# Performance work log

Hardware: AMD Instinct MI355X
Metric: run time of the kernel (lower is better)

Reference implementation:

```python
import jax, jax.numpy as jnp
import numpy as np
import math

BATCH = 32
F_IN, F_OUT = 16, 32
B_IN, B_OUT = 16, 8
N_SPEC = B_OUT * (4 * B_OUT ** 2 - 1) // 3  # sum_{l<b_out} (2l+1)^2 = 680
ALPHAS = [2.0 * np.pi * a / 6.0 for a in range(6)]
GAMMAS = [2.0 * np.pi * c / 4.0 for c in range(4)]
GRID = [(al, np.pi / 16.0, ga) for al in ALPHAS for ga in GAMMAS]  # 24 (alpha, beta, gamma) points
SCALING = 1.0 / math.sqrt(len(GRID) * F_IN * B_OUT ** 3 / B_IN ** 3)


def _wigner_d(l, beta):
    """Wigner small-d matrix d^l_{m'm}(beta), centered order m',m=-l..l, quantum/Condon-Shortley."""
    lg = math.lgamma
    cb, sb = math.cos(beta / 2.0), math.sin(beta / 2.0)
    d = np.zeros((2 * l + 1, 2 * l + 1))
    for i, mp in enumerate(range(-l, l + 1)):
        for j, m in enumerate(range(-l, l + 1)):
            pref = 0.5 * (lg(l + mp + 1) + lg(l - mp + 1) + lg(l + m + 1) + lg(l - m + 1))
            tot = 0.0
            for s in range(max(0, m - mp), min(l + m, l - mp) + 1):
                den = lg(l + m - s + 1) + lg(s + 1) + lg(mp - m + s + 1) + lg(l - mp - s + 1)
                tot += ((-1.0) ** (mp - m + s) * math.exp(pref - den)
                        * cb ** (2 * l + m - mp - 2 * s) * sb ** (mp - m + 2 * s))
            d[i, j] = tot
    return d


def _quad_weights(b):
    """SOFT quadrature weights at beta_j = pi(2j+1)/(4b); 1/(2b)^2 absorbs the unnormalized 2D FFT."""
    k = np.arange(b)
    j = np.arange(2 * b)
    w = (2.0 / b) * np.sin(np.pi * (2 * j + 1) / (4.0 * b)) * (
        np.sin(np.pi * np.outer(2 * j + 1, 2 * k + 1) / (4.0 * b)) / (2 * k + 1)).sum(axis=1)
    return w / (2 * b) ** 2


def _setup_tables():
    betas_in = np.pi * (2 * np.arange(2 * B_IN) + 1) / (4.0 * B_IN)
    betas_out = np.pi * (2 * np.arange(2 * B_OUT) + 1) / (4.0 * B_OUT)
    w = _quad_weights(B_IN)
    wig_fwd = np.stack([np.concatenate([w[j] * _wigner_d(l, b).ravel() for l in range(B_OUT)])
                        for j, b in enumerate(betas_in)])          # [2*B_IN, N_SPEC]
    wig_inv = np.stack([np.concatenate([(2 * l + 1) * _wigner_d(l, b).ravel() for l in range(B_OUT)])
                        for b in betas_out])                       # [2*B_OUT, N_SPEC]
    F = np.zeros((len(GRID), N_SPEC), dtype=np.complex128)
    for p, (al, be, ga) in enumerate(GRID):
        blocks = []
        for l in range(B_OUT):
            m = np.arange(-l, l + 1)
            D = np.exp(-1j * m[:, None] * al) * _wigner_d(l, be) * np.exp(-1j * m[None, :] * ga)
            blocks.append(np.conj(D).ravel())
        F[p] = np.concatenate(blocks)
    return (wig_fwd.astype(np.float32), wig_inv.astype(np.float32),
            F.real.astype(np.float32), F.imag.astype(np.float32))


def _freq_idx(l, n):
    # packed frequencies -l..-1,0..l with wraparound into an FFT axis of length n
    return np.r_[np.arange(n - l, n), np.arange(l + 1)] if l > 0 else np.arange(1)


def _forward(x, kernel, bias, wigner_fwd, wigner_inv, ft_re, ft_im):
    xf = jnp.fft.fft2(x)  # FFT over (alpha, gamma): [B, Fin, 2b_in, 2b_in, 2b_in] complex64
    # SO3_fft_real: weighted Wigner-d contraction over beta, per degree l
    xhat = []
    for l in range(B_OUT):
        idx = _freq_idx(l, 2 * B_IN)
        xx = xf[:, :, :, idx[:, None], idx[None, :]]  # [B, Fin, beta, 2l+1, 2l+1]
        s0 = l * (4 * l * l - 1) // 3
        wl = wigner_fwd[:, s0:s0 + (2 * l + 1) ** 2].reshape(2 * B_IN, 2 * l + 1, 2 * l + 1)
        xhat.append(jnp.einsum('bmn,zfbmn->mnzf', wl, xx))  # [2l+1, 2l+1, B, Fin]
    # so3_rft of the scaled kernel on the grid: yhat [N_SPEC, Fin, Fout]
    Fc = ft_re + 1j * ft_im  # [P, N_SPEC]
    yhat = jnp.einsum('iop,ps->sio', (kernel * SCALING).astype(jnp.complex64), Fc)
    # so3_mm: per-degree z^l = x^l (y^l)^H, then inverse SO3 FFT
    B = x.shape[0]
    ff = jnp.zeros((B, F_OUT, 2 * B_OUT, 2 * B_OUT, 2 * B_OUT), dtype=xf.dtype)
    for l in range(B_OUT):
        s0 = l * (4 * l * l - 1) // 3
        yl = yhat[s0:s0 + (2 * l + 1) ** 2].reshape(2 * l + 1, 2 * l + 1, F_IN, F_OUT)
        zl = jnp.einsum('mkzf,nkfg->mnzg', xhat[l], jnp.conj(yl))  # [2l+1, 2l+1, B, Fout]
        wl = wigner_inv[:, s0:s0 + (2 * l + 1) ** 2].reshape(2 * B_OUT, 2 * l + 1, 2 * l + 1)
        o = jnp.einsum('mnzg,bmn->zgbmn', zl, wl)  # [B, Fout, beta_out, 2l+1, 2l+1]
        idx = _freq_idx(l, 2 * B_OUT)
        ff = ff.at[:, :, :, idx[:, None], idx[None, :]].add(o)
    out = jnp.real(jnp.fft.ifft2(ff)) * float((2 * B_OUT) ** 2)  # undo ifft 1/N^2, keep real part
    return out + bias


def setup_inputs():
    key = jax.random.key(0)
    k1, k2 = jax.random.split(key)
    x = jax.random.normal(k1, (BATCH, F_IN, 2 * B_IN, 2 * B_IN, 2 * B_IN), dtype=jnp.float32)
    kernel = jax.random.uniform(k2, (F_IN, F_OUT, len(GRID)), minval=-1.0, maxval=1.0, dtype=jnp.float32)
    bias = jnp.zeros((1, F_OUT, 1, 1, 1), jnp.float32)
    wf, wi, fre, fim = _setup_tables()
    return {"x": x, "kernel": kernel, "bias": bias,
            "wigner_fwd": jnp.asarray(wf), "wigner_inv": jnp.asarray(wi),
            "ft_re": jnp.asarray(fre), "ft_im": jnp.asarray(fim)}


def reference(x, kernel, bias, wigner_fwd, wigner_inv, ft_re, ft_im):
    return _forward(x, kernel, bias, wigner_fwd, wigner_inv, ft_re, ft_im)
```

## Files before the change

### kernel.cpp

```cpp
#include <hip/hip_runtime.h>
#include <math.h>


#define NS 680
#define NR 372
#define NP 24
#define NW 15
#define SLB 4
#define SCALING 0.14433756729740643f

__device__ __constant__ int c_s0[9] = {0, 1, 10, 35, 84, 165, 286, 455, 680};
__device__ __constant__ int c_o[9]  = {0, 1, 7, 22, 50, 95, 161, 252, 372};

__device__ __constant__ float2 TW32[32] = {
    { 1.0000000000f,  0.0000000000f}, { 0.9807852804f, -0.1950903220f},
    { 0.9238795325f, -0.3826834324f}, { 0.8314696123f, -0.5555702330f},
    { 0.7071067812f, -0.7071067812f}, { 0.5555702330f, -0.8314696123f},
    { 0.3826834324f, -0.9238795325f}, { 0.1950903220f, -0.9807852804f},
    { 0.0000000000f, -1.0000000000f}, {-0.1950903220f, -0.9807852804f},
    {-0.3826834324f, -0.9238795325f}, {-0.5555702330f, -0.8314696123f},
    {-0.7071067812f, -0.7071067812f}, {-0.8314696123f, -0.5555702330f},
    {-0.9238795325f, -0.3826834324f}, {-0.9807852804f, -0.1950903220f},
    {-1.0000000000f,  0.0000000000f}, {-0.9807852804f,  0.1950903220f},
    {-0.9238795325f,  0.3826834324f}, {-0.8314696123f,  0.5555702330f},
    {-0.7071067812f,  0.7071067812f}, {-0.5555702330f,  0.8314696123f},
    {-0.3826834324f,  0.9238795325f}, {-0.1950903220f,  0.9807852804f},
    { 0.0000000000f,  1.0000000000f}, { 0.1950903220f,  0.9807852804f},
    { 0.3826834324f,  0.9238795325f}, { 0.5555702330f,  0.8314696123f},
    { 0.7071067812f,  0.7071067812f}, { 0.8314696123f,  0.5555702330f},
    { 0.9238795325f,  0.3826834324f}, { 0.9807852804f,  0.1950903220f}};

__device__ __constant__ float2 TW16P[16] = {
    { 1.0000000000f,  0.0000000000f}, { 0.9238795325f,  0.3826834324f},
    { 0.7071067812f,  0.7071067812f}, { 0.3826834324f,  0.9238795325f},
    { 0.0000000000f,  1.0000000000f}, {-0.3826834324f,  0.9238795325f},
    {-0.7071067812f,  0.7071067812f}, {-0.9238795325f,  0.3826834324f},
    {-1.0000000000f,  0.0000000000f}, {-0.9238795325f, -0.3826834324f},
    {-0.7071067812f, -0.7071067812f}, {-0.3826834324f, -0.9238795325f},
    { 0.0000000000f, -1.0000000000f}, { 0.3826834324f, -0.9238795325f},
    { 0.7071067812f, -0.7071067812f}, { 0.9238795325f, -0.3826834324f}};

__global__ __launch_bounds__(256) void A12(const float* __restrict__ x,
                                           float2* __restrict__ xf2) {
    __shared__ __align__(16) float  sx[SLB * 1152];
    __shared__ __align__(16) float2 st[SLB][8][34];
    __shared__ float2 tw[32];
    int blk = blockIdx.x;
    int tid = threadIdx.x;
    if (tid < 32) tw[tid] = TW32[tid];
    {
        const float4* xs = (const float4*)(x + (size_t)blk * (SLB * 1024));
#pragma unroll
        for (int q = 0; q < SLB; q++) {
            int idx = q * 256 + tid;
            float4 v4 = xs[idx];
            int sl = idx >> 8, w = idx & 255;
            *(float4*)&sx[sl * 1152 + (w >> 3) * 36 + (w & 7) * 4] = v4;
        }
    }
    __syncthreads();
    {
        int u = tid >> 3, n = tid & 7;
        float sgn = (n & 1) ? -1.f : 1.f;
        float2 t8[8];
#pragma unroll
        for (int c = 0; c < 8; c++) t8[c] = tw[(n * c) & 31];
        float2 fa1 = tw[(8 * n) & 31];
#pragma unroll
        for (int sl = 0; sl < SLB; sl++) {
            const float* row = &sx[sl * 1152 + u * 36];
            float4 x0 = *(float4*)&row[0],  x1 = *(float4*)&row[4];
            float4 x2 = *(float4*)&row[8],  x3 = *(float4*)&row[12];
            float4 x4 = *(float4*)&row[16], x5 = *(float4*)&row[20];
            float4 x6 = *(float4*)&row[24], x7 = *(float4*)&row[28];
            float y0  = fmaf(sgn, x4.x, x0.x), y1  = fmaf(sgn, x4.y, x0.y);
            float y2  = fmaf(sgn, x4.z, x0.z), y3  = fmaf(sgn, x4.w, x0.w);
            float y4  = fmaf(sgn, x5.x, x1.x), y5  = fmaf(sgn, x5.y, x1.y);
            float y6  = fmaf(sgn, x5.z, x1.z), y7  = fmaf(sgn, x5.w, x1.w);
            float y8  = fmaf(sgn, x6.x, x2.x), y9  = fmaf(sgn, x6.y, x2.y);
            float y10 = fmaf(sgn, x6.z, x2.z), y11 = fmaf(sgn, x6.w, x2.w);
            float y12 = fmaf(sgn, x7.x, x3.x), y13 = fmaf(sgn, x7.y, x3.y);
            float y14 = fmaf(sgn, x7.z, x3.z), y15 = fmaf(sgn, x7.w, x3.w);
            float p0r = y0 * t8[0].x + y1 * t8[1].x + y2 * t8[2].x + y3 * t8[3].x
                      + y4 * t8[4].x + y5 * t8[5].x + y6 * t8[6].x + y7 * t8[7].x;
            float p0i = y0 * t8[0].y + y1 * t8[1].y + y2 * t8[2].y + y3 * t8[3].y
                      + y4 * t8[4].y + y5 * t8[5].y + y6 * t8[6].y + y7 * t8[7].y;
            float p1r = y8 * t8[0].x + y9 * t8[1].x + y10 * t8[2].x + y11 * t8[3].x
                      + y12 * t8[4].x + y13 * t8[5].x + y14 * t8[6].x + y15 * t8[7].x;
            float p1i = y8 * t8[0].y + y9 * t8[1].y + y10 * t8[2].y + y11 * t8[3].y
                      + y12 * t8[4].y + y13 * t8[5].y + y14 * t8[6].y + y15 * t8[7].y;
            float re = p0r + fa1.x * p1r - fa1.y * p1i;
            float im = p0i + fa1.x * p1i + fa1.y * p1r;
            st[sl][n][u] = make_float2(re, im);
        }
    }
    __syncthreads();
    {
        int sl = tid >> 6, m = (tid >> 3) & 7, jj = tid & 7;
        float2 t8[8], fa[4];
#pragma unroll
        for (int c = 0; c < 8; c++) t8[c] = tw[(m * c) & 31];
        fa[0] = make_float2(1.f, 0.f);
#pragma unroll
        for (int a = 1; a < 4; a++) fa[a] = tw[(8 * m * a) & 31];
        float reP = 0.f, imP = 0.f, reN = 0.f, imN = 0.f;
#pragma unroll
        for (int a = 0; a < 4; a++) {
            const float4* spt = (const float4*)&st[sl][jj][a * 8];
            float4 r0 = spt[0], r1 = spt[1], r2 = spt[2], r3 = spt[3];
            float A = r0.x * t8[0].x + r0.z * t8[1].x + r1.x * t8[2].x + r1.z * t8[3].x
                    + r2.x * t8[4].x + r2.z * t8[5].x + r3.x * t8[6].x + r3.z * t8[7].x;
            float B = r0.y * t8[0].y + r0.w * t8[1].y + r1.y * t8[2].y + r1.w * t8[3].y
                    + r2.y * t8[4].y + r2.w * t8[5].y + r3.y * t8[6].y + r3.w * t8[7].y;
            float C = r0.x * t8[0].y + r0.z * t8[1].y + r1.x * t8[2].y + r1.z * t8[3].y
                    + r2.x * t8[4].y + r2.z * t8[5].y + r3.x * t8[6].y + r3.z * t8[7].y;
            float D = r0.y * t8[0].x + r0.w * t8[1].x + r1.y * t8[2].x + r1.w * t8[3].x
                    + r2.y * t8[4].x + r2.w * t8[5].x + r3.y * t8[6].x + r3.w * t8[7].x;
            float prP = A - B, piP = C + D;
            float prN = A + B, piN = C - D;
            reP += fa[a].x * prP - fa[a].y * piP;
            imP += fa[a].x * piP + fa[a].y * prP;
            reN += fa[a].x * prN - fa[a].y * piN;
            imN += fa[a].x * piN + fa[a].y * prN;
        }
        int slice = blk * SLB + sl;
        float2* ob = xf2 + (size_t)slice * 120 + m * 15;
        ob[7 + jj] = make_float2(reP, imP);
        if (jj) ob[7 - jj] = make_float2(reN, imN);
    }
}

__global__ void kP(const float* __restrict__ kern, const float* __restrict__ fre,
                   const float* __restrict__ fim, const float* __restrict__ wf,
                   const float* __restrict__ wi, float2* __restrict__ yhat,
                   float* __restrict__ wfT, float* __restrict__ wiTd) {
    int idx = blockIdx.x * blockDim.x + threadIdx.x;
    if (idx < NS * 512) {
        int s = idx >> 9, fg = idx & 511;
        float re = 0.f, im = 0.f;
        for (int p = 0; p < NP; p++) {
            float kv = kern[fg * NP + p];
            re += kv * fre[p * NS + s];
            im += kv * fim[p * NS + s];
        }
        yhat[(size_t)s * 512 + fg] = make_float2(re * SCALING, im * SCALING);
        return;
    }
    int j = idx - NS * 512;
    if (j < NR * 32) {
        int sp = j >> 5, b = j & 31;
        int l = 0;
#pragma unroll
        for (int t = 1; t < 8; t++) if (sp >= c_o[t]) l = t;
        int K = 2 * l + 1, r = sp - c_o[l];
        int m = r / K, jn = r - m * K;
        int sf = c_s0[l] + (m + l) * K + jn;
        wfT[sp * 32 + b] = wf[b * NS + sf];
        return;
    }
    int k = j - NR * 32;
    if (k >= 16384) return;
    int ni = k & 15, mm = (k >> 4) & 7, b8 = (k >> 7) & 7;
    int l = (k >> 10) & 7, bh = k >> 13;
    int nn = ni - 7;
    float v = 0.f;
    if (ni < 15 && mm <= l && nn >= -l && nn <= l) {
        int K = 2 * l + 1;
        v = wi[(bh * 8 + b8) * NS + c_s0[l] + (mm + l) * K + (nn + l)];
    }
    wiTd[k] = v;
}

__global__ __launch_bounds__(256) void A3(const float2* __restrict__ xf2,
                                          const float* __restrict__ wfT,
                                          float2* __restrict__ xhat) {
    __shared__ __align__(16) float2 sxf[32 * 120];
    int zf = blockIdx.x;
    int tid = threadIdx.x;
    {
        const float4* src = (const float4*)(xf2 + (size_t)zf * (32 * 120));
        float4* dst = (float4*)sxf;
        for (int t = tid; t < 32 * 60; t += 256) dst[t] = src[t];
    }
    __syncthreads();
#pragma unroll
    for (int q = 0; q < 2; q++) {
        if (q == 1 && tid >= NR - 256) break;
        int sp = tid + q * 256;
        int l = 0;
#pragma unroll
        for (int t = 1; t < 8; t++) if (sp >= c_o[t]) l = t;
        int K = 2 * l + 1, r = sp - c_o[l];
        int m = r / K, jn = r - m * K;
        int cell = m * 15 + (jn - l + 7);
        const float4* wp = (const float4*)(wfT + sp * 32);
        const float2* xp = sxf + cell;
        float re = 0.f, im = 0.f;
#pragma unroll
        for (int qq = 0; qq < 8; qq++) {
            float4 w4 = wp[qq];
            float2 v0 = xp[(qq * 4 + 0) * 120];
            float2 v1 = xp[(qq * 4 + 1) * 120];
            float2 v2 = xp[(qq * 4 + 2) * 120];
            float2 v3 = xp[(qq * 4 + 3) * 120];
            re += w4.x * v0.x + w4.y * v1.x + w4.z * v2.x + w4.w * v3.x;
            im += w4.x * v0.y + w4.y * v1.y + w4.z * v2.y + w4.w * v3.y;
        }
        xhat[(size_t)sp * 512 + zf] = make_float2(re, im);
    }
}

__global__ __launch_bounds__(512) void kD(const float2* __restrict__ xhat,
                                          const float2* __restrict__ yhat,
                                          float2* __restrict__ zbufT) {
    __shared__ __align__(16) float2 Xs[4][16][34];
    __shared__ __align__(16) float2 Ys[4][16][34];
    int sp = 371 - blockIdx.x;
    int l = 0;
#pragma unroll
    for (int t = 1; t < 8; t++) if (sp >= c_o[t]) l = t;
    int K = 2 * l + 1, r = sp - c_o[l];
    int m = r / K, jn = r - m * K;
    int sX0 = c_o[l] + m * K;
    int sY0 = c_s0[l] + jn * K;
    int tid = threadIdx.x;
    int zl = tid >> 4;
    int g0 = (tid & 15) * 2;
    float2 acc0 = make_float2(0.f, 0.f), acc1 = make_float2(0.f, 0.f);
    int nchunks = (K + 3) >> 2;
    for (int chunk = 0; chunk < nchunks; ++chunk) {
#pragma unroll
        for (int kw = 0; kw < 4; kw++) {
            int k = chunk * 4 + kw;
            if (k < K)
                Xs[kw][tid & 15][tid >> 4] =
                    xhat[(size_t)(sX0 + k) * 512 + (tid >> 4) * 16 + (tid & 15)];
        }
#pragma unroll
        for (int kw = 0; kw < 4; kw++) {
            int k = chunk * 4 + kw;
            if (k < K)
                Ys[kw][tid >> 5][tid & 31] = yhat[(size_t)(sY0 + k) * 512 + tid];
        }
        __syncthreads();
#pragma unroll
        for (int kw = 0; kw < 4; kw++) {
            int k = chunk * 4 + kw;
            if (k < K) {
#pragma unroll
                for (int f = 0; f < 16; f++) {
                    float2 xv = Xs[kw][f][zl];
                    float4 y4 = *(const float4*)&Ys[kw][f][g0];
                    acc0.x += xv.x * y4.x + xv.y * y4.y;
                    acc0.y += xv.y * y4.x - xv.x * y4.y;
                    acc1.x += xv.x * y4.z + xv.y * y4.w;
                    acc1.y += xv.y * y4.z - xv.x * y4.w;
                }
            }
        }
        __syncthreads();
    }
    zbufT[(size_t)(zl * 32 + g0) * NR + sp]     = acc0;
    zbufT[(size_t)(zl * 32 + g0 + 1) * NR + sp] = acc1;
}

__global__ __launch_bounds__(256) void kE4(const float2* __restrict__ zbufT,
                                           const float* __restrict__ wiTd,
                                           const float* __restrict__ bias,
                                           float* __restrict__ out) {
    __shared__ float2 szp[384];
    __shared__ float2 g1[16 * 139];
    __shared__ float2 tw[16];
    int zg = blockIdx.x;
    int g = zg & 31;
    int tid = threadIdx.x;
    if (tid < 16) tw[tid] = TW16P[tid];
    if (tid < 8)    szp[tid] = make_float2(0.f, 0.f);
    if (tid >= 252) szp[tid + 128] = make_float2(0.f, 0.f);
    for (int t = tid; t < NR; t += 256) szp[8 + t] = zbufT[(size_t)zg * NR + t];
    __syncthreads();
    {
        int b = tid & 15, mm = (tid >> 4) & 7, vh = tid >> 7;
        int bh = b >> 3, b8 = b & 7;
        const int co[8] = {0, 1, 7, 22, 50, 95, 161, 252};
        float2 ff[15];
#pragma unroll
        for (int n = 0; n < 15; n++) ff[n] = make_float2(0.f, 0.f);
#pragma unroll
        for (int l = 0; l < 8; l++) {
            const float4* wl = (const float4*)(wiTd + ((((bh * 8 + l) * 8 + b8) * 8 + mm) << 4));
            float4 w0 = wl[0], w1 = wl[1], w2 = wl[2], w3 = wl[3];
            float wreg[16] = {w0.x, w0.y, w0.z, w0.w, w1.x, w1.y, w1.z, w1.w,
                              w2.x, w2.y, w2.z, w2.w, w3.x, w3.y, w3.z, w3.w};
            int sp = 1 + co[l] + mm * (2 * l + 1) + l;
#pragma unroll
            for (int ni = 0; ni < 15; ni++) {
                float w = wreg[ni];
                float2 v = szp[sp + ni];
                ff[ni].x += w * v.x; ff[ni].y += w * v.y;
            }
        }
#pragma unroll
        for (int j = 0; j < 8; j++) {
            int v = vh * 8 + j;
            float re = 0.f, im = 0.f;
#pragma unroll
            for (int n = 0; n < 15; n++) {
                float2 c = tw[((n - 7) * v) & 15];
                float2 a = ff[n];
                re += a.x * c.x - a.y * c.y;
                im += a.x * c.y + a.y * c.x;
            }
            g1[b * 139 + mm * 17 + v] = make_float2(re, im);
        }
    }
    __syncthreads();
    {
        int b = tid & 15, u = tid >> 4;
        float o[16];
#pragma unroll
        for (int j = 0; j < 16; j++) o[j] = g1[b * 139 + j].x;
#pragma unroll
        for (int m = 1; m < 8; m++) {
            float2 c = tw[(m * u) & 15];
#pragma unroll
            for (int j = 0; j < 16; j++) {
                float2 a = g1[b * 139 + m * 17 + j];
                o[j] += 2.f * (a.x * c.x - a.y * c.y);
            }
        }
        float bv = bias[g];
        float* ob = out + ((size_t)zg * 16 + b) * 256 + u * 16;
#pragma unroll
        for (int j = 0; j < 16; j += 4)
            *(float4*)&ob[j] = make_float4(o[j] + bv, o[j + 1] + bv, o[j + 2] + bv, o[j + 3] + bv);
    }
}

extern "C" void kernel_launch(void* const* d_in, const int* in_sizes, int n_in,
                              void* d_out, int out_size, void* d_ws, size_t ws_size,
                              hipStream_t stream) {
    const float* x    = (const float*)d_in[0];
    const float* kern = (const float*)d_in[1];
    const float* bias = (const float*)d_in[2];
    const float* wf   = (const float*)d_in[3];
    const float* wi   = (const float*)d_in[4];
    const float* fre  = (const float*)d_in[5];
    const float* fim  = (const float*)d_in[6];
    float* out = (float*)d_out;

    char* ws = (char*)d_ws;
    float2* xf2   = (float2*)ws;
    float2* xhat  = (float2*)(ws + 15728640);
    float2* yhat  = (float2*)(ws + 17252352);
    float2* zbufT = (float2*)(ws + 20037632);
    float*  wfT   = (float*)(ws + 23085056);
    float*  wiTd  = (float*)(ws + 23132672);

    A12<<<4096, 256, 0, stream>>>(x, xf2);
    kP<<<1471, 256, 0, stream>>>(kern, fre, fim, wf, wi, yhat, wfT, wiTd);
    A3<<<512, 256, 0, stream>>>(xf2, wfT, xhat);
    kD<<<372, 512, 0, stream>>>(xhat, yhat, zbufT);
    kE4<<<1024, 256, 0, stream>>>(zbufT, wiTd, bias, out);
}
```

Baseline: 90.94 us.

## Merge kernel-prep into the FFT launch and split kD blocks across batch halves

Folds the independent kP table-preparation kernel into the A12 FFT kernel as extra blocks, so both run in a single launch and can overlap. kD now launches two 256-thread blocks per spectral index, each handling half the batch, which doubles the block count for better CU occupancy. In exchange, every yhat tile is loaded twice, and the fused kernel carries the larger register and shared-memory footprint of the FFT path for the prep blocks too.

```diff
diff --git a/kernel.cpp b/kernel.cpp
--- a/kernel.cpp
+++ b/kernel.cpp
@@ -40,13 +40,60 @@
     { 0.0000000000f, -1.0000000000f}, { 0.3826834324f, -0.9238795325f},
     { 0.7071067812f, -0.7071067812f}, { 0.9238795325f, -0.3826834324f}};
 
-__global__ __launch_bounds__(256) void A12(const float* __restrict__ x,
-                                           float2* __restrict__ xf2) {
+__global__ __launch_bounds__(256) void A12P(const float* __restrict__ x,
+                                            const float* __restrict__ kern,
+                                            const float* __restrict__ fre,
+                                            const float* __restrict__ fim,
+                                            const float* __restrict__ wf,
+                                            const float* __restrict__ wi,
+                                            float2* __restrict__ xf2,
+                                            float2* __restrict__ yhat,
+                                            float* __restrict__ wfT,
+                                            float* __restrict__ wiTd) {
     __shared__ __align__(16) float  sx[SLB * 1152];
     __shared__ __align__(16) float2 st[SLB][8][34];
     __shared__ float2 tw[32];
-    int blk = blockIdx.x;
+    int bid = blockIdx.x;
     int tid = threadIdx.x;
+    if (bid >= 4096) {
+        int idx = (bid - 4096) * 256 + tid;
+        if (idx < NS * 512) {
+            int s = idx >> 9, fg = idx & 511;
+            float re = 0.f, im = 0.f;
+            for (int p = 0; p < NP; p++) {
+                float kv = kern[fg * NP + p];
+                re += kv * fre[p * NS + s];
+                im += kv * fim[p * NS + s];
+            }
+            yhat[(size_t)s * 512 + fg] = make_float2(re * SCALING, im * SCALING);
+            return;
+        }
+        int j = idx - NS * 512;
+        if (j < NR * 32) {
+            int sp = j >> 5, b = j & 31;
+            int l = 0;
+#pragma unroll
+            for (int t = 1; t < 8; t++) if (sp >= c_o[t]) l = t;
+            int K = 2 * l + 1, r = sp - c_o[l];
+            int m = r / K, jn = r - m * K;
+            int sf = c_s0[l] + (m + l) * K + jn;
+            wfT[sp * 32 + b] = wf[b * NS + sf];
+            return;
+        }
+        int k = j - NR * 32;
+        if (k >= 16384) return;
+        int ni = k & 15, mm = (k >> 4) & 7, b8 = (k >> 7) & 7;
+        int l = (k >> 10) & 7, bh = k >> 13;
+        int nn = ni - 7;
+        float v = 0.f;
+        if (ni < 15 && mm <= l && nn >= -l && nn <= l) {
+            int K = 2 * l + 1;
+            v = wi[(bh * 8 + b8) * NS + c_s0[l] + (mm + l) * K + (nn + l)];
+        }
+        wiTd[k] = v;
+        return;
+    }
+    int blk = bid;
     if (tid < 32) tw[tid] = TW32[tid];
     {
         const float4* xs = (const float4*)(x + (size_t)blk * (SLB * 1024));
@@ -130,47 +177,6 @@
     }
 }
 
-__global__ void kP(const float* __restrict__ kern, const float* __restrict__ fre,
-                   const float* __restrict__ fim, const float* __restrict__ wf,
-                   const float* __restrict__ wi, float2* __restrict__ yhat,
-                   float* __restrict__ wfT, float* __restrict__ wiTd) {
-    int idx = blockIdx.x * blockDim.x + threadIdx.x;
-    if (idx < NS * 512) {
-        int s = idx >> 9, fg = idx & 511;
-        float re = 0.f, im = 0.f;
-        for (int p = 0; p < NP; p++) {
-            float kv = kern[fg * NP + p];
-            re += kv * fre[p * NS + s];
-            im += kv * fim[p * NS + s];
-        }
-        yhat[(size_t)s * 512 + fg] = make_float2(re * SCALING, im * SCALING);
-        return;
-    }
-    int j = idx - NS * 512;
-    if (j < NR * 32) {
-        int sp = j >> 5, b = j & 31;
-        int l = 0;
-#pragma unroll
-        for (int t = 1; t < 8; t++) if (sp >= c_o[t]) l = t;
-        int K = 2 * l + 1, r = sp - c_o[l];
-        int m = r / K, jn = r - m * K;
-        int sf = c_s0[l] + (m + l) * K + jn;
-        wfT[sp * 32 + b] = wf[b * NS + sf];
-        return;
-    }
-    int k = j - NR * 32;
-    if (k >= 16384) return;
-    int ni = k & 15, mm = (k >> 4) & 7, b8 = (k >> 7) & 7;
-    int l = (k >> 10) & 7, bh = k >> 13;
-    int nn = ni - 7;
-    float v = 0.f;
-    if (ni < 15 && mm <= l && nn >= -l && nn <= l) {
-        int K = 2 * l + 1;
-        v = wi[(bh * 8 + b8) * NS + c_s0[l] + (mm + l) * K + (nn + l)];
-    }
-    wiTd[k] = v;
-}
-
 __global__ __launch_bounds__(256) void A3(const float2* __restrict__ xf2,
                                           const float* __restrict__ wfT,
                                           float2* __restrict__ xhat) {
@@ -210,12 +216,13 @@
     }
 }
 
-__global__ __launch_bounds__(512) void kD(const float2* __restrict__ xhat,
+__global__ __launch_bounds__(256) void kD(const float2* __restrict__ xhat,
                                           const float2* __restrict__ yhat,
                                           float2* __restrict__ zbufT) {
-    __shared__ __align__(16) float2 Xs[4][16][34];
+    __shared__ __align__(16) float2 Xs[4][16][18];
     __shared__ __align__(16) float2 Ys[4][16][34];
-    int sp = 371 - blockIdx.x;
+    int sp = 371 - (blockIdx.x >> 1);
+    int zh = blockIdx.x & 1;
     int l = 0;
 #pragma unroll
     for (int t = 1; t < 8; t++) if (sp >= c_o[t]) l = t;
@@ -234,13 +241,15 @@
             int k = chunk * 4 + kw;
             if (k < K)
                 Xs[kw][tid & 15][tid >> 4] =
-                    xhat[(size_t)(sX0 + k) * 512 + (tid >> 4) * 16 + (tid & 15)];
-        }
-#pragma unroll
-        for (int kw = 0; kw < 4; kw++) {
+                    xhat[(size_t)(sX0 + k) * 512 + (zh * 16 + (tid >> 4)) * 16 + (tid & 15)];
+        }
+#pragma unroll
+        for (int it = 0; it < 8; it++) {
+            int kw = it >> 1;
+            int fg = (it & 1) * 256 + tid;
             int k = chunk * 4 + kw;
             if (k < K)
-                Ys[kw][tid >> 5][tid & 31] = yhat[(size_t)(sY0 + k) * 512 + tid];
+                Ys[kw][fg >> 5][fg & 31] = yhat[(size_t)(sY0 + k) * 512 + fg];
         }
         __syncthreads();
 #pragma unroll
@@ -260,8 +269,9 @@
         }
         __syncthreads();
     }
-    zbufT[(size_t)(zl * 32 + g0) * NR + sp]     = acc0;
-    zbufT[(size_t)(zl * 32 + g0 + 1) * NR + sp] = acc1;
+    int z0 = zh * 16 + zl;
+    zbufT[(size_t)(z0 * 32 + g0) * NR + sp]     = acc0;
+    zbufT[(size_t)(z0 * 32 + g0 + 1) * NR + sp] = acc1;
 }
 
 __global__ __launch_bounds__(256) void kE4(const float2* __restrict__ zbufT,
@@ -357,9 +367,8 @@
     float*  wfT   = (float*)(ws + 23085056);
     float*  wiTd  = (float*)(ws + 23132672);
 
-    A12<<<4096, 256, 0, stream>>>(x, xf2);
-    kP<<<1471, 256, 0, stream>>>(kern, fre, fim, wf, wi, yhat, wfT, wiTd);
+    A12P<<<5567, 256, 0, stream>>>(x, kern, fre, fim, wf, wi, xf2, yhat, wfT, wiTd);
     A3<<<512, 256, 0, stream>>>(xf2, wfT, xhat);
-    kD<<<372, 512, 0, stream>>>(xhat, yhat, zbufT);
+    kD<<<744, 256, 0, stream>>>(xhat, yhat, zbufT);
     kE4<<<1024, 256, 0, stream>>>(zbufT, wiTd, bias, out);
 }
```

After: 81.60 us. -10.3%, faster.
